# Kernel tuning notes

Hardware: AMD Instinct MI355X
Metric: run time of the kernel (lower is better)

## Reference

```python
import jax, jax.numpy as jnp
import numpy as np

N_NODES = 50000
N_EDGES = 600000
IN_C = 128
HID = 128
OUT_C = 32
N_GRAPHS = 64


def setup_inputs() -> dict:
    key = jax.random.key(0)
    ks = jax.random.split(key, 12)
    x = jax.random.normal(ks[0], (N_NODES, IN_C), dtype=jnp.float32)
    edge_index = jax.random.randint(ks[1], (2, N_EDGES), 0, N_NODES, dtype=jnp.int64)
    batch = jnp.sort(jax.random.randint(ks[2], (N_NODES,), 0, N_GRAPHS, dtype=jnp.int64))
    s1 = 1.0 / np.sqrt(IN_C)
    s2 = 1.0 / np.sqrt(HID)
    # SAGEConv: out = lin_l(mean_neighbors) + lin_r(x); lin_l has bias, lin_r has none
    W1l = jax.random.uniform(ks[3], (HID, IN_C), minval=-s1, maxval=s1, dtype=jnp.float32)
    b1 = jax.random.uniform(ks[4], (HID,), minval=-s1, maxval=s1, dtype=jnp.float32)
    W1r = jax.random.uniform(ks[5], (HID, IN_C), minval=-s1, maxval=s1, dtype=jnp.float32)
    W2l = jax.random.uniform(ks[6], (HID, HID), minval=-s2, maxval=s2, dtype=jnp.float32)
    b2 = jax.random.uniform(ks[7], (HID,), minval=-s2, maxval=s2, dtype=jnp.float32)
    W2r = jax.random.uniform(ks[8], (HID, HID), minval=-s2, maxval=s2, dtype=jnp.float32)
    Wlin = jax.random.uniform(ks[9], (OUT_C, HID), minval=-s2, maxval=s2, dtype=jnp.float32)
    blin = jax.random.uniform(ks[10], (OUT_C,), minval=-s2, maxval=s2, dtype=jnp.float32)
    return {"x": x, "edge_index": edge_index, "batch": batch,
            "W1l": W1l, "b1": b1, "W1r": W1r,
            "W2l": W2l, "b2": b2, "W2r": W2r,
            "Wlin": Wlin, "blin": blin}


def _sage_conv(x, src, dst, Wl, bl, Wr):
    # mean aggregation of source-node features onto destination nodes
    msg_sum = jax.ops.segment_sum(x[src], dst, num_segments=N_NODES)  # [N, d]
    deg = jax.ops.segment_sum(jnp.ones((src.shape[0],), x.dtype), dst, num_segments=N_NODES)
    mean = msg_sum / jnp.maximum(deg, 1.0)[:, None]
    return mean @ Wl.T + bl + x @ Wr.T


def reference(x, edge_index, batch, W1l, b1, W1r, W2l, b2, W2r, Wlin, blin):
    src, dst = edge_index[0], edge_index[1]
    h = jax.nn.relu(_sage_conv(x, src, dst, W1l, b1, W1r))
    h = jax.nn.relu(_sage_conv(h, src, dst, W2l, b2, W2r))
    # global mean pool over graph ids
    gsum = jax.ops.segment_sum(h, batch, num_segments=N_GRAPHS)        # [G, HID]
    cnt = jax.ops.segment_sum(jnp.ones((h.shape[0],), h.dtype), batch, num_segments=N_GRAPHS)
    pooled = gsum / jnp.maximum(cnt, 1.0)[:, None]
    return pooled @ Wlin.T + blin
```

## Files before the change

kernel.cpp:

```cpp
#include <hip/hip_runtime.h>
#include <hip/hip_fp16.h>

#define N_NODES 50000
#define N_EDGES 600000
#define N_GRAPHS 64
#define HID 128
#define OUT_C 32

#define SCAN_BLK 256
#define N_SCAN_BLOCKS ((N_NODES + SCAN_BLK - 1) / SCAN_BLK)

typedef __attribute__((ext_vector_type(8))) _Float16 half8;
typedef __attribute__((ext_vector_type(4))) float f32x4;

__global__ void build_w_f16(const float* __restrict__ Wlw, const float* __restrict__ Wrw,
                            __half* __restrict__ Wh, __half* __restrict__ Wl) {
    int idx = blockIdx.x * 256 + threadIdx.x;
    int n = idx >> 8, k = idx & 255;
    float a = (k < 128) ? Wlw[n * 128 + k] : Wrw[n * 128 + (k - 128)];
    __half hh = __float2half(a);
    float hf = __half2float(hh);
    Wh[idx] = hh;
    Wl[idx] = __float2half(a - hf);
}

__global__ void cast_f16(const float* __restrict__ in, __half* __restrict__ out, int n) {
    int i = (blockIdx.x * 256 + threadIdx.x) * 4;
    if (i < n) {
        float4 v = *(const float4*)(in + i);
        __half2 a = __floats2half2_rn(v.x, v.y);
        __half2 b = __floats2half2_rn(v.z, v.w);
        uint2 st;
        st.x = *(const unsigned int*)&a;
        st.y = *(const unsigned int*)&b;
        *(uint2*)(out + i) = st;
    }
}

__global__ void deg_kernel(const int* __restrict__ dst, int* __restrict__ deg, int E) {
    int e = blockIdx.x * 256 + threadIdx.x;
    if (e < E) atomicAdd(&deg[dst[e]], 1);
}

__global__ __launch_bounds__(SCAN_BLK) void scan_blocksum(
    const int* __restrict__ deg, int* __restrict__ bsum) {
    __shared__ int s[SCAN_BLK];
    int i = blockIdx.x * SCAN_BLK + threadIdx.x;
    s[threadIdx.x] = (i < N_NODES) ? deg[i] : 0;
    __syncthreads();
    for (int off = SCAN_BLK / 2; off > 0; off >>= 1) {
        if (threadIdx.x < off) s[threadIdx.x] += s[threadIdx.x + off];
        __syncthreads();
    }
    if (threadIdx.x == 0) bsum[blockIdx.x] = s[0];
}

__global__ __launch_bounds__(256) void scan_boff(
    const int* __restrict__ bsum, int* __restrict__ boff, int* __restrict__ rowptr) {
    __shared__ int s[256];
    int t = threadIdx.x;
    int v = (t < N_SCAN_BLOCKS) ? bsum[t] : 0;
    s[t] = v;
    __syncthreads();
    for (int off = 1; off < 256; off <<= 1) {
        int u = (t >= off) ? s[t - off] : 0;
        __syncthreads();
        s[t] += u;
        __syncthreads();
    }
    if (t < N_SCAN_BLOCKS) boff[t] = s[t] - v;
    if (t == N_SCAN_BLOCKS - 1) rowptr[N_NODES] = s[t];
}

__global__ __launch_bounds__(SCAN_BLK) void scan_emit(
    const int* __restrict__ deg, const int* __restrict__ boff,
    int* __restrict__ rowptr, float* __restrict__ invdeg) {
    __shared__ int s[SCAN_BLK];
    int i = blockIdx.x * SCAN_BLK + threadIdx.x;
    int t = threadIdx.x;
    int v = (i < N_NODES) ? deg[i] : 0;
    s[t] = v;
    __syncthreads();
    for (int off = 1; off < SCAN_BLK; off <<= 1) {
        int u = (t >= off) ? s[t - off] : 0;
        __syncthreads();
        s[t] += u;
        __syncthreads();
    }
    if (i < N_NODES) {
        rowptr[i] = boff[blockIdx.x] + s[t] - v;
        invdeg[i] = 1.0f / fmaxf((float)v, 1.0f);
    }
}

__global__ void fill_kernel(const int* __restrict__ src, const int* __restrict__ dst,
                            const int* __restrict__ rowptr, int* __restrict__ cursor,
                            int* __restrict__ eidx, int E) {
    int e = blockIdx.x * 256 + threadIdx.x;
    if (e < E) {
        int d = dst[e];
        int pos = atomicAdd(&cursor[d], 1);
        eidx[rowptr[d] + pos] = src[e];
    }
}

__global__ __launch_bounds__(256) void aggregate_f16(
    const __half* __restrict__ feat16, const int* __restrict__ rowptr,
    const int* __restrict__ eidx, const float* __restrict__ invdeg,
    __half* __restrict__ mean16) {
    const int node = blockIdx.x * 4 + (threadIdx.x >> 6);
    if (node >= N_NODES) return;
    const int lane = threadIdx.x & 63;
    const int beg = rowptr[node];
    const int end = rowptr[node + 1];
    const size_t coff = (size_t)lane * 2;

    float2 a0 = {0.f, 0.f}, a1 = {0.f, 0.f}, a2 = {0.f, 0.f}, a3 = {0.f, 0.f};
    int i = beg;
    for (; i + 8 <= end; i += 8) {
        int s0 = eidx[i + 0], s1 = eidx[i + 1], s2 = eidx[i + 2], s3 = eidx[i + 3];
        int s4 = eidx[i + 4], s5 = eidx[i + 5], s6 = eidx[i + 6], s7 = eidx[i + 7];
        __half2 v0 = *(const __half2*)(feat16 + (size_t)s0 * 128 + coff);
        __half2 v1 = *(const __half2*)(feat16 + (size_t)s1 * 128 + coff);
        __half2 v2 = *(const __half2*)(feat16 + (size_t)s2 * 128 + coff);
        __half2 v3 = *(const __half2*)(feat16 + (size_t)s3 * 128 + coff);
        __half2 v4 = *(const __half2*)(feat16 + (size_t)s4 * 128 + coff);
        __half2 v5 = *(const __half2*)(feat16 + (size_t)s5 * 128 + coff);
        __half2 v6 = *(const __half2*)(feat16 + (size_t)s6 * 128 + coff);
        __half2 v7 = *(const __half2*)(feat16 + (size_t)s7 * 128 + coff);
        float2 f0 = __half22float2(v0), f1 = __half22float2(v1);
        float2 f2 = __half22float2(v2), f3 = __half22float2(v3);
        float2 f4 = __half22float2(v4), f5 = __half22float2(v5);
        float2 f6 = __half22float2(v6), f7 = __half22float2(v7);
        a0.x += f0.x; a0.y += f0.y;  a1.x += f1.x; a1.y += f1.y;
        a2.x += f2.x; a2.y += f2.y;  a3.x += f3.x; a3.y += f3.y;
        a0.x += f4.x; a0.y += f4.y;  a1.x += f5.x; a1.y += f5.y;
        a2.x += f6.x; a2.y += f6.y;  a3.x += f7.x; a3.y += f7.y;
    }
    if (i + 4 <= end) {
        int s0 = eidx[i + 0], s1 = eidx[i + 1], s2 = eidx[i + 2], s3 = eidx[i + 3];
        __half2 v0 = *(const __half2*)(feat16 + (size_t)s0 * 128 + coff);
        __half2 v1 = *(const __half2*)(feat16 + (size_t)s1 * 128 + coff);
        __half2 v2 = *(const __half2*)(feat16 + (size_t)s2 * 128 + coff);
        __half2 v3 = *(const __half2*)(feat16 + (size_t)s3 * 128 + coff);
        float2 f0 = __half22float2(v0), f1 = __half22float2(v1);
        float2 f2 = __half22float2(v2), f3 = __half22float2(v3);
        a0.x += f0.x; a0.y += f0.y;  a1.x += f1.x; a1.y += f1.y;
        a2.x += f2.x; a2.y += f2.y;  a3.x += f3.x; a3.y += f3.y;
        i += 4;
    }
    if (i + 2 <= end) {
        int s0 = eidx[i + 0], s1 = eidx[i + 1];
        __half2 v0 = *(const __half2*)(feat16 + (size_t)s0 * 128 + coff);
        __half2 v1 = *(const __half2*)(feat16 + (size_t)s1 * 128 + coff);
        float2 f0 = __half22float2(v0), f1 = __half22float2(v1);
        a0.x += f0.x; a0.y += f0.y;  a1.x += f1.x; a1.y += f1.y;
        i += 2;
    }
    if (i < end) {
        int s0 = eidx[i];
        float2 f0 = __half22float2(*(const __half2*)(feat16 + (size_t)s0 * 128 + coff));
        a0.x += f0.x; a0.y += f0.y;
    }

    const float sc = invdeg[node];
    float mx = ((a0.x + a1.x) + (a2.x + a3.x)) * sc;
    float my = ((a0.y + a1.y) + (a2.y + a3.y)) * sc;
    *(__half2*)(mean16 + (size_t)node * 128 + lane * 2) = __floats2half2_rn(mx, my);
}

#define GBM 64
#define BSTR 48

__global__ __launch_bounds__(256) void sage_gemm_f16(
    const __half* __restrict__ mean16, const __half* __restrict__ feat16,
    const __half* __restrict__ Wh, const __half* __restrict__ Wl,
    const float* __restrict__ bias, __half* __restrict__ out16, int M) {
    __shared__ __align__(16) __half Bh[128][BSTR];
    __shared__ __align__(16) __half Bl[128][BSTR];

    const int tid = threadIdx.x;
    const int wave = tid >> 6;
    const int lane = tid & 63;
    const int l15 = lane & 15;
    const int quad = lane >> 4;
    const int row0 = blockIdx.x * GBM;
    const int gi_a = min(row0 + wave * 16 + l15, M - 1);

    half8 af[8];
#pragma unroll
    for (int kb = 0; kb < 8; ++kb) {
        const int k0 = kb * 32;
        const __half* ap = (k0 < 128)
            ? (mean16 + (size_t)gi_a * 128 + k0 + quad * 8)
            : (feat16 + (size_t)gi_a * 128 + (k0 - 128) + quad * 8);
        af[kb] = *(const half8*)ap;
    }

    f32x4 acc[8];
#pragma unroll
    for (int t = 0; t < 8; ++t) acc[t] = (f32x4){0.f, 0.f, 0.f, 0.f};

#pragma unroll
    for (int kb = 0; kb < 8; ++kb) {
        const int k0 = kb * 32;
#pragma unroll
        for (int i = 0; i < 2; ++i) {
            int id = tid + i * 256;
            int n = id >> 2;
            int kc = (id & 3) * 8;
            *(half8*)&Bh[n][kc] = *(const half8*)(Wh + (size_t)n * 256 + k0 + kc);
            *(half8*)&Bl[n][kc] = *(const half8*)(Wl + (size_t)n * 256 + k0 + kc);
        }
        __syncthreads();

#pragma unroll
        for (int t = 0; t < 8; ++t) {
            const half8 b_h = *(const half8*)&Bh[t * 16 + l15][quad * 8];
            const half8 b_l = *(const half8*)&Bl[t * 16 + l15][quad * 8];
            acc[t] = __builtin_amdgcn_mfma_f32_16x16x32_f16(af[kb], b_h, acc[t], 0, 0, 0);
            acc[t] = __builtin_amdgcn_mfma_f32_16x16x32_f16(af[kb], b_l, acc[t], 0, 0, 0);
        }
        __syncthreads();
    }

#pragma unroll
    for (int r = 0; r < 4; ++r) {
        int gi = row0 + wave * 16 + quad * 4 + r;
        if (gi < M) {
#pragma unroll
            for (int t = 0; t < 8; ++t) {
                int col = t * 16 + l15;
                float v = fmaxf(acc[t][r] + bias[col], 0.f);
                out16[(size_t)gi * 128 + col] = __float2half(v);
            }
        }
    }
}

#define POOL_PARTS 4
__global__ __launch_bounds__(256) void pool_graph(
    const __half* __restrict__ h, const int* __restrict__ batch,
    float* __restrict__ pooled, int* __restrict__ gcnt) {
    const int g = blockIdx.x >> 2;
    const int part = blockIdx.x & 3;
    int lo = 0, hi = N_NODES;
    while (lo < hi) { int mid = (lo + hi) >> 1; if (batch[mid] < g) lo = mid + 1; else hi = mid; }
    const int start = lo;
    hi = N_NODES;
    while (lo < hi) { int mid = (lo + hi) >> 1; if (batch[mid] < g + 1) lo = mid + 1; else hi = mid; }
    const int end = lo;

    const int t = threadIdx.x;
    if (part == 0 && t == 0) gcnt[g] = end - start;

    const int c4 = (t & 31) * 4;
    const int rg = t >> 5;
    float4 acc = {0.f, 0.f, 0.f, 0.f};
    for (int n = start + part * 8 + rg; n < end; n += 8 * POOL_PARTS) {
        const __half2* p = (const __half2*)(h + (size_t)n * 128 + c4);
        float2 f0 = __half22float2(p[0]);
        float2 f1 = __half22float2(p[1]);
        acc.x += f0.x; acc.y += f0.y; acc.z += f1.x; acc.w += f1.y;
    }
    __shared__ float sm[8][132];
    sm[rg][c4 + 0] = acc.x;
    sm[rg][c4 + 1] = acc.y;
    sm[rg][c4 + 2] = acc.z;
    sm[rg][c4 + 3] = acc.w;
    __syncthreads();
    if (t < 128) {
        float s = 0.f;
#pragma unroll
        for (int r = 0; r < 8; ++r) s += sm[r][t];
        atomicAdd(&pooled[g * 128 + t], s);
    }
}

__global__ void final_kernel(const float* __restrict__ pooled, const int* __restrict__ gcnt,
                             const float* __restrict__ Wlin, const float* __restrict__ blin,
                             float* __restrict__ out) {
    int g = blockIdx.x;
    int j = threadIdx.x;
    float inv = 1.0f / fmaxf((float)gcnt[g], 1.0f);
    float sum = blin[j];
    const float* prow = pooled + g * 128;
    const float* wrow = Wlin + j * 128;
    for (int c = 0; c < 128; ++c) sum += prow[c] * inv * wrow[c];
    out[g * 32 + j] = sum;
}

extern "C" void kernel_launch(void* const* d_in, const int* in_sizes, int n_in,
                              void* d_out, int out_size, void* d_ws, size_t ws_size,
                              hipStream_t stream) {
    const float* x    = (const float*)d_in[0];
    const int*   src  = (const int*)d_in[1];
    const int*   dst  = ((const int*)d_in[1]) + N_EDGES;
    const int*   batch= (const int*)d_in[2];
    const float* W1l  = (const float*)d_in[3];
    const float* b1   = (const float*)d_in[4];
    const float* W1r  = (const float*)d_in[5];
    const float* W2l  = (const float*)d_in[6];
    const float* b2   = (const float*)d_in[7];
    const float* W2r  = (const float*)d_in[8];
    const float* Wlin = (const float*)d_in[9];
    const float* blin = (const float*)d_in[10];
    float* out = (float*)d_out;

    __half* xh     = (__half*)d_ws;
    __half* mean16 = xh + 6400000;
    __half* h1_16  = mean16 + 6400000;
    __half* h2_16  = h1_16 + 6400000;
    __half* Wh1    = h2_16 + 6400000;
    __half* Wl1    = Wh1 + 32768;
    __half* Wh2    = Wl1 + 32768;
    __half* Wl2    = Wh2 + 32768;
    float* pooled  = (float*)(Wl2 + 32768);
    int*   gcnt    = (int*)(pooled + N_GRAPHS * 128);
    float* invdeg  = (float*)(gcnt + 64);
    int*   degi    = (int*)(invdeg + N_NODES);
    int*   cursor  = degi + N_NODES;
    int*   rowptr  = cursor + N_NODES;
    int*   eidx    = rowptr + N_NODES + 1;
    int*   bsum    = eidx + N_EDGES;
    int*   boff    = bsum + N_SCAN_BLOCKS;

    hipMemsetAsync(degi, 0, (size_t)(2 * N_NODES) * sizeof(int), stream);
    hipMemsetAsync(pooled, 0, (size_t)(N_GRAPHS * 128) * sizeof(float), stream);

    build_w_f16<<<128, 256, 0, stream>>>(W1l, W1r, Wh1, Wl1);
    build_w_f16<<<128, 256, 0, stream>>>(W2l, W2r, Wh2, Wl2);
    cast_f16<<<(N_NODES * 128 / 4 + 255) / 256, 256, 0, stream>>>(x, xh, N_NODES * 128);

    deg_kernel<<<(N_EDGES + 255) / 256, 256, 0, stream>>>(dst, degi, N_EDGES);
    scan_blocksum<<<N_SCAN_BLOCKS, SCAN_BLK, 0, stream>>>(degi, bsum);
    scan_boff<<<1, 256, 0, stream>>>(bsum, boff, rowptr);
    scan_emit<<<N_SCAN_BLOCKS, SCAN_BLK, 0, stream>>>(degi, boff, rowptr, invdeg);
    fill_kernel<<<(N_EDGES + 255) / 256, 256, 0, stream>>>(src, dst, rowptr, cursor, eidx, N_EDGES);

    const int gemm_grid = (N_NODES + GBM - 1) / GBM;

    aggregate_f16<<<(N_NODES + 3) / 4, 256, 0, stream>>>(xh, rowptr, eidx, invdeg, mean16);
    sage_gemm_f16<<<gemm_grid, 256, 0, stream>>>(mean16, xh, Wh1, Wl1, b1, h1_16, N_NODES);

    aggregate_f16<<<(N_NODES + 3) / 4, 256, 0, stream>>>(h1_16, rowptr, eidx, invdeg, mean16);
    sage_gemm_f16<<<gemm_grid, 256, 0, stream>>>(mean16, h1_16, Wh2, Wl2, b2, h2_16, N_NODES);

    pool_graph<<<N_GRAPHS * POOL_PARTS, 256, 0, stream>>>(h2_16, batch, pooled, gcnt);
    final_kernel<<<N_GRAPHS, 32, 0, stream>>>(pooled, gcnt, Wlin, blin, out);
}
```

Baseline: 272.3 us.

## Drop split-f16 weight correction, stage full weights once, widen aggregate loads

Removes the low-order f16 weight residual, which halves the MFMA count in the SAGE GEMM at some cost in accuracy. The whole 128x256 weight matrix is loaded into LDS once per block, replacing the per-K-slice staging that needed two barriers per step. The aggregation kernel now gives each half-wave one node and loads half4 instead of half2, doubling the bytes per gather. The weight build and the x cast are merged into a single launch.

```diff
diff --git a/kernel.cpp b/kernel.cpp
--- a/kernel.cpp
+++ b/kernel.cpp
@@ -11,29 +11,37 @@
 #define N_SCAN_BLOCKS ((N_NODES + SCAN_BLK - 1) / SCAN_BLK)
 
 typedef __attribute__((ext_vector_type(8))) _Float16 half8;
+typedef __attribute__((ext_vector_type(4))) _Float16 half4;
 typedef __attribute__((ext_vector_type(4))) float f32x4;
 
-__global__ void build_w_f16(const float* __restrict__ Wlw, const float* __restrict__ Wrw,
-                            __half* __restrict__ Wh, __half* __restrict__ Wl) {
-    int idx = blockIdx.x * 256 + threadIdx.x;
-    int n = idx >> 8, k = idx & 255;
-    float a = (k < 128) ? Wlw[n * 128 + k] : Wrw[n * 128 + (k - 128)];
-    __half hh = __float2half(a);
-    float hf = __half2float(hh);
-    Wh[idx] = hh;
-    Wl[idx] = __float2half(a - hf);
-}
-
-__global__ void cast_f16(const float* __restrict__ in, __half* __restrict__ out, int n) {
-    int i = (blockIdx.x * 256 + threadIdx.x) * 4;
-    if (i < n) {
-        float4 v = *(const float4*)(in + i);
-        __half2 a = __floats2half2_rn(v.x, v.y);
-        __half2 b = __floats2half2_rn(v.z, v.w);
-        uint2 st;
-        st.x = *(const unsigned int*)&a;
-        st.y = *(const unsigned int*)&b;
-        *(uint2*)(out + i) = st;
+__global__ __launch_bounds__(256) void prep_kernel(
+    const float* __restrict__ x,
+    const float* __restrict__ W1l, const float* __restrict__ W1r,
+    const float* __restrict__ W2l, const float* __restrict__ W2r,
+    __half* __restrict__ xh, __half* __restrict__ Wt1, __half* __restrict__ Wt2) {
+    int b = blockIdx.x;
+    if (b < 16) {
+        int idx = b * 256 + threadIdx.x;
+        for (int i = idx; i < 65536; i += 4096) {
+            int which = i >> 15;
+            int j = i & 32767;
+            int n = j >> 8, k = j & 255;
+            const float* Wl = which ? W2l : W1l;
+            const float* Wr = which ? W2r : W1r;
+            float a = (k < 128) ? Wl[n * 128 + k] : Wr[n * 128 + (k - 128)];
+            (which ? Wt2 : Wt1)[j] = __float2half(a);
+        }
+    } else {
+        int i = ((b - 16) * 256 + threadIdx.x) * 4;
+        if (i < N_NODES * 128) {
+            float4 v = *(const float4*)(x + i);
+            __half2 a = __floats2half2_rn(v.x, v.y);
+            __half2 b2 = __floats2half2_rn(v.z, v.w);
+            uint2 st;
+            st.x = *(const unsigned int*)&a;
+            st.y = *(const unsigned int*)&b2;
+            *(uint2*)(xh + i) = st;
+        }
     }
 }
 
@@ -104,80 +112,81 @@
     }
 }
 
+#define AGG_ACC(vv, aa) { aa.x += (float)vv[0]; aa.y += (float)vv[1]; \
+                          aa.z += (float)vv[2]; aa.w += (float)vv[3]; }
+
 __global__ __launch_bounds__(256) void aggregate_f16(
     const __half* __restrict__ feat16, const int* __restrict__ rowptr,
     const int* __restrict__ eidx, const float* __restrict__ invdeg,
     __half* __restrict__ mean16) {
-    const int node = blockIdx.x * 4 + (threadIdx.x >> 6);
-    if (node >= N_NODES) return;
+    const int wave = threadIdx.x >> 6;
     const int lane = threadIdx.x & 63;
-    const int beg = rowptr[node];
-    const int end = rowptr[node + 1];
-    const size_t coff = (size_t)lane * 2;
-
-    float2 a0 = {0.f, 0.f}, a1 = {0.f, 0.f}, a2 = {0.f, 0.f}, a3 = {0.f, 0.f};
+    const int nh   = lane >> 5;
+    const int sub  = lane & 31;
+    const int node = blockIdx.x * 8 + wave * 2 + nh;
+    const bool act = (node < N_NODES);
+    int beg = 0, end = 0;
+    if (act) { beg = rowptr[node]; end = rowptr[node + 1]; }
+    const size_t coff = (size_t)sub * 4;
+
+    float4 a0 = {0.f,0.f,0.f,0.f}, a1 = {0.f,0.f,0.f,0.f};
+    float4 a2 = {0.f,0.f,0.f,0.f}, a3 = {0.f,0.f,0.f,0.f};
     int i = beg;
     for (; i + 8 <= end; i += 8) {
-        int s0 = eidx[i + 0], s1 = eidx[i + 1], s2 = eidx[i + 2], s3 = eidx[i + 3];
-        int s4 = eidx[i + 4], s5 = eidx[i + 5], s6 = eidx[i + 6], s7 = eidx[i + 7];
-        __half2 v0 = *(const __half2*)(feat16 + (size_t)s0 * 128 + coff);
-        __half2 v1 = *(const __half2*)(feat16 + (size_t)s1 * 128 + coff);
-        __half2 v2 = *(const __half2*)(feat16 + (size_t)s2 * 128 + coff);
-        __half2 v3 = *(const __half2*)(feat16 + (size_t)s3 * 128 + coff);
-        __half2 v4 = *(const __half2*)(feat16 + (size_t)s4 * 128 + coff);
-        __half2 v5 = *(const __half2*)(feat16 + (size_t)s5 * 128 + coff);
-        __half2 v6 = *(const __half2*)(feat16 + (size_t)s6 * 128 + coff);
-        __half2 v7 = *(const __half2*)(feat16 + (size_t)s7 * 128 + coff);
-        float2 f0 = __half22float2(v0), f1 = __half22float2(v1);
-        float2 f2 = __half22float2(v2), f3 = __half22float2(v3);
-        float2 f4 = __half22float2(v4), f5 = __half22float2(v5);
-        float2 f6 = __half22float2(v6), f7 = __half22float2(v7);
-        a0.x += f0.x; a0.y += f0.y;  a1.x += f1.x; a1.y += f1.y;
-        a2.x += f2.x; a2.y += f2.y;  a3.x += f3.x; a3.y += f3.y;
-        a0.x += f4.x; a0.y += f4.y;  a1.x += f5.x; a1.y += f5.y;
-        a2.x += f6.x; a2.y += f6.y;  a3.x += f7.x; a3.y += f7.y;
+        int s0 = eidx[i+0], s1 = eidx[i+1], s2 = eidx[i+2], s3 = eidx[i+3];
+        int s4 = eidx[i+4], s5 = eidx[i+5], s6 = eidx[i+6], s7 = eidx[i+7];
+        half4 v0 = *(const half4*)(feat16 + (size_t)s0 * 128 + coff);
+        half4 v1 = *(const half4*)(feat16 + (size_t)s1 * 128 + coff);
+        half4 v2 = *(const half4*)(feat16 + (size_t)s2 * 128 + coff);
+        half4 v3 = *(const half4*)(feat16 + (size_t)s3 * 128 + coff);
+        half4 v4 = *(const half4*)(feat16 + (size_t)s4 * 128 + coff);
+        half4 v5 = *(const half4*)(feat16 + (size_t)s5 * 128 + coff);
+        half4 v6 = *(const half4*)(feat16 + (size_t)s6 * 128 + coff);
+        half4 v7 = *(const half4*)(feat16 + (size_t)s7 * 128 + coff);
+        AGG_ACC(v0, a0); AGG_ACC(v1, a1); AGG_ACC(v2, a2); AGG_ACC(v3, a3);
+        AGG_ACC(v4, a0); AGG_ACC(v5, a1); AGG_ACC(v6, a2); AGG_ACC(v7, a3);
     }
     if (i + 4 <= end) {
-        int s0 = eidx[i + 0], s1 = eidx[i + 1], s2 = eidx[i + 2], s3 = eidx[i + 3];
-        __half2 v0 = *(const __half2*)(feat16 + (size_t)s0 * 128 + coff);
-        __half2 v1 = *(const __half2*)(feat16 + (size_t)s1 * 128 + coff);
-        __half2 v2 = *(const __half2*)(feat16 + (size_t)s2 * 128 + coff);
-        __half2 v3 = *(const __half2*)(feat16 + (size_t)s3 * 128 + coff);
-        float2 f0 = __half22float2(v0), f1 = __half22float2(v1);
-        float2 f2 = __half22float2(v2), f3 = __half22float2(v3);
-        a0.x += f0.x; a0.y += f0.y;  a1.x += f1.x; a1.y += f1.y;
-        a2.x += f2.x; a2.y += f2.y;  a3.x += f3.x; a3.y += f3.y;
+        int s0 = eidx[i+0], s1 = eidx[i+1], s2 = eidx[i+2], s3 = eidx[i+3];
+        half4 v0 = *(const half4*)(feat16 + (size_t)s0 * 128 + coff);
+        half4 v1 = *(const half4*)(feat16 + (size_t)s1 * 128 + coff);
+        half4 v2 = *(const half4*)(feat16 + (size_t)s2 * 128 + coff);
+        half4 v3 = *(const half4*)(feat16 + (size_t)s3 * 128 + coff);
+        AGG_ACC(v0, a0); AGG_ACC(v1, a1); AGG_ACC(v2, a2); AGG_ACC(v3, a3);
         i += 4;
     }
     if (i + 2 <= end) {
-        int s0 = eidx[i + 0], s1 = eidx[i + 1];
-        __half2 v0 = *(const __half2*)(feat16 + (size_t)s0 * 128 + coff);
-        __half2 v1 = *(const __half2*)(feat16 + (size_t)s1 * 128 + coff);
-        float2 f0 = __half22float2(v0), f1 = __half22float2(v1);
-        a0.x += f0.x; a0.y += f0.y;  a1.x += f1.x; a1.y += f1.y;
+        int s0 = eidx[i+0], s1 = eidx[i+1];
+        half4 v0 = *(const half4*)(feat16 + (size_t)s0 * 128 + coff);
+        half4 v1 = *(const half4*)(feat16 + (size_t)s1 * 128 + coff);
+        AGG_ACC(v0, a0); AGG_ACC(v1, a1);
         i += 2;
     }
     if (i < end) {
         int s0 = eidx[i];
-        float2 f0 = __half22float2(*(const __half2*)(feat16 + (size_t)s0 * 128 + coff));
-        a0.x += f0.x; a0.y += f0.y;
-    }
-
-    const float sc = invdeg[node];
-    float mx = ((a0.x + a1.x) + (a2.x + a3.x)) * sc;
-    float my = ((a0.y + a1.y) + (a2.y + a3.y)) * sc;
-    *(__half2*)(mean16 + (size_t)node * 128 + lane * 2) = __floats2half2_rn(mx, my);
+        half4 v0 = *(const half4*)(feat16 + (size_t)s0 * 128 + coff);
+        AGG_ACC(v0, a0);
+    }
+
+    if (act) {
+        const float sc = invdeg[node];
+        half4 r;
+        r[0] = (_Float16)(((a0.x + a1.x) + (a2.x + a3.x)) * sc);
+        r[1] = (_Float16)(((a0.y + a1.y) + (a2.y + a3.y)) * sc);
+        r[2] = (_Float16)(((a0.z + a1.z) + (a2.z + a3.z)) * sc);
+        r[3] = (_Float16)(((a0.w + a1.w) + (a2.w + a3.w)) * sc);
+        *(half4*)(mean16 + (size_t)node * 128 + coff) = r;
+    }
 }
 
 #define GBM 64
-#define BSTR 48
+#define BPAD 8
 
 __global__ __launch_bounds__(256) void sage_gemm_f16(
     const __half* __restrict__ mean16, const __half* __restrict__ feat16,
-    const __half* __restrict__ Wh, const __half* __restrict__ Wl,
-    const float* __restrict__ bias, __half* __restrict__ out16, int M) {
-    __shared__ __align__(16) __half Bh[128][BSTR];
-    __shared__ __align__(16) __half Bl[128][BSTR];
+    const __half* __restrict__ Wt, const float* __restrict__ bias,
+    __half* __restrict__ out16, int M) {
+    __shared__ __align__(16) __half Bs[128][256 + BPAD];
 
     const int tid = threadIdx.x;
     const int wave = tid >> 6;
@@ -187,6 +196,12 @@
     const int row0 = blockIdx.x * GBM;
     const int gi_a = min(row0 + wave * 16 + l15, M - 1);
 
+    for (int id = tid; id < 128 * 32; id += 256) {
+        int n = id >> 5;
+        int kc = (id & 31) * 8;
+        *(half8*)&Bs[n][kc] = *(const half8*)(Wt + (size_t)n * 256 + kc);
+    }
+
     half8 af[8];
 #pragma unroll
     for (int kb = 0; kb < 8; ++kb) {
@@ -201,27 +216,15 @@
 #pragma unroll
     for (int t = 0; t < 8; ++t) acc[t] = (f32x4){0.f, 0.f, 0.f, 0.f};
 
+    __syncthreads();
+
 #pragma unroll
     for (int kb = 0; kb < 8; ++kb) {
-        const int k0 = kb * 32;
-#pragma unroll
-        for (int i = 0; i < 2; ++i) {
-            int id = tid + i * 256;
-            int n = id >> 2;
-            int kc = (id & 3) * 8;
-            *(half8*)&Bh[n][kc] = *(const half8*)(Wh + (size_t)n * 256 + k0 + kc);
-            *(half8*)&Bl[n][kc] = *(const half8*)(Wl + (size_t)n * 256 + k0 + kc);
+#pragma unroll
+        for (int t = 0; t < 8; ++t) {
+            const half8 b = *(const half8*)&Bs[t * 16 + l15][kb * 32 + quad * 8];
+            acc[t] = __builtin_amdgcn_mfma_f32_16x16x32_f16(af[kb], b, acc[t], 0, 0, 0);
         }
-        __syncthreads();
-
-#pragma unroll
-        for (int t = 0; t < 8; ++t) {
-            const half8 b_h = *(const half8*)&Bh[t * 16 + l15][quad * 8];
-            const half8 b_l = *(const half8*)&Bl[t * 16 + l15][quad * 8];
-            acc[t] = __builtin_amdgcn_mfma_f32_16x16x32_f16(af[kb], b_h, acc[t], 0, 0, 0);
-            acc[t] = __builtin_amdgcn_mfma_f32_16x16x32_f16(af[kb], b_l, acc[t], 0, 0, 0);
-        }
-        __syncthreads();
     }
 
 #pragma unroll
@@ -311,11 +314,9 @@
     __half* mean16 = xh + 6400000;
     __half* h1_16  = mean16 + 6400000;
     __half* h2_16  = h1_16 + 6400000;
-    __half* Wh1    = h2_16 + 6400000;
-    __half* Wl1    = Wh1 + 32768;
-    __half* Wh2    = Wl1 + 32768;
-    __half* Wl2    = Wh2 + 32768;
-    float* pooled  = (float*)(Wl2 + 32768);
+    __half* Wt1    = h2_16 + 6400000;
+    __half* Wt2    = Wt1 + 32768;
+    float* pooled  = (float*)(Wt2 + 32768);
     int*   gcnt    = (int*)(pooled + N_GRAPHS * 128);
     float* invdeg  = (float*)(gcnt + 64);
     int*   degi    = (int*)(invdeg + N_NODES);
@@ -328,9 +329,8 @@
     hipMemsetAsync(degi, 0, (size_t)(2 * N_NODES) * sizeof(int), stream);
     hipMemsetAsync(pooled, 0, (size_t)(N_GRAPHS * 128) * sizeof(float), stream);
 
-    build_w_f16<<<128, 256, 0, stream>>>(W1l, W1r, Wh1, Wl1);
-    build_w_f16<<<128, 256, 0, stream>>>(W2l, W2r, Wh2, Wl2);
-    cast_f16<<<(N_NODES * 128 / 4 + 255) / 256, 256, 0, stream>>>(x, xh, N_NODES * 128);
+    prep_kernel<<<16 + (N_NODES * 128 / 4 + 255) / 256, 256, 0, stream>>>(
+        x, W1l, W1r, W2l, W2r, xh, Wt1, Wt2);
 
     deg_kernel<<<(N_EDGES + 255) / 256, 256, 0, stream>>>(dst, degi, N_EDGES);
     scan_blocksum<<<N_SCAN_BLOCKS, SCAN_BLK, 0, stream>>>(degi, bsum);
@@ -339,12 +339,13 @@
     fill_kernel<<<(N_EDGES + 255) / 256, 256, 0, stream>>>(src, dst, rowptr, cursor, eidx, N_EDGES);
 
     const int gemm_grid = (N_NODES + GBM - 1) / GBM;
-
-    aggregate_f16<<<(N_NODES + 3) / 4, 256, 0, stream>>>(xh, rowptr, eidx, invdeg, mean16);
-    sage_gemm_f16<<<gemm_grid, 256, 0, stream>>>(mean16, xh, Wh1, Wl1, b1, h1_16, N_NODES);
-
-    aggregate_f16<<<(N_NODES + 3) / 4, 256, 0, stream>>>(h1_16, rowptr, eidx, invdeg, mean16);
-    sage_gemm_f16<<<gemm_grid, 256, 0, stream>>>(mean16, h1_16, Wh2, Wl2, b2, h2_16, N_NODES);
+    const int agg_grid = (N_NODES + 7) / 8;
+
+    aggregate_f16<<<agg_grid, 256, 0, stream>>>(xh, rowptr, eidx, invdeg, mean16);
+    sage_gemm_f16<<<gemm_grid, 256, 0, stream>>>(mean16, xh, Wt1, b1, h1_16, N_NODES);
+
+    aggregate_f16<<<agg_grid, 256, 0, stream>>>(h1_16, rowptr, eidx, invdeg, mean16);
+    sage_gemm_f16<<<gemm_grid, 256, 0, stream>>>(mean16, h1_16, Wt2, b2, h2_16, N_NODES);
 
     pool_graph<<<N_GRAPHS * POOL_PARTS, 256, 0, stream>>>(h2_16, batch, pooled, gcnt);
     final_kernel<<<N_GRAPHS, 32, 0, stream>>>(pooled, gcnt, Wlin, blin, out);
```

Result: faster. 263.8 us (-3.1%).
